# Optimization experiments

Hardware: AMD Instinct MI355X
Metric: run time of the kernel (lower is better)

Reference implementation:

```python
import jax, jax.numpy as jnp
import numpy as np

N = 50000
E = 800000
F_IN = 64
HID = 64


def setup_inputs() -> dict:
    key = jax.random.key(0)
    k1, k2, k3, k4, k5, k6 = jax.random.split(key, 6)
    x = jax.random.normal(k1, (N, F_IN), dtype=jnp.float32)
    edge_index = jax.random.randint(k2, (2, E), 0, N, dtype=jnp.int64)
    # GraphSAGE mean-aggregator layers: Linear(2*in -> out) applied to [x || mean_agg(x)]
    W1 = jax.random.normal(k3, (2 * F_IN, HID), dtype=jnp.float32) / np.sqrt(2 * F_IN)
    b1 = jnp.zeros((HID,), dtype=jnp.float32)
    W2 = jax.random.normal(k4, (2 * HID, HID), dtype=jnp.float32) / np.sqrt(2 * HID)
    b2 = jnp.zeros((HID,), dtype=jnp.float32)
    return {"x": x, "edge_index": edge_index, "W1": W1, "b1": b1, "W2": W2, "b2": b2}


def _sage_conv(x, src, dst, W, b):
    # mean aggregation of neighbor (src) features at dst, then linear on [self || agg]
    msg = x[src]                                                   # [E, d] gather
    s = jax.ops.segment_sum(msg, dst, num_segments=N)              # [N, d]
    cnt = jax.ops.segment_sum(jnp.ones((src.shape[0], 1), x.dtype), dst, num_segments=N)
    agg = s / jnp.maximum(cnt, 1.0)
    return jnp.concatenate([x, agg], axis=-1) @ W + b


def reference(x, edge_index, W1, b1, W2, b2):
    src, dst = edge_index[0], edge_index[1]
    h = _sage_conv(x, src, dst, W1, b1)
    h = jax.nn.relu(h)  # dropout is identity at inference
    h = _sage_conv(h, src, dst, W2, b2)
    return h
```

## Files before the change

kernel.cpp:

```cpp
#include <hip/hip_runtime.h>

#define N_NODES 50000
#define N_EDGES 800000
#define F 64
#define CHUNK 6144
#define NWG1 ((N_EDGES + CHUNK - 1) / CHUNK)
#define NBUCK 196
#define CAP2 8192
#define NWTILE (N_NODES / 16)

typedef __attribute__((ext_vector_type(8))) _Float16 half8;
typedef __attribute__((ext_vector_type(4))) float f32x4;

__global__ __launch_bounds__(256) void conv_hist(
    const float4* __restrict__ xin,
    half8*        __restrict__ x16,
    const int*    __restrict__ dst,
    int*          __restrict__ bhist,
    const float*  __restrict__ W1, const float* __restrict__ W2,
    _Float16*     __restrict__ Wt1, _Float16* __restrict__ Wt2) {
  int t = threadIdx.x, b = blockIdx.x;
  if (b == NWG1) {
    for (int i = t; i < 64 * 128; i += 256) {
      int n = i >> 7, k = i & 127;
      Wt1[i] = (_Float16)W1[k * 64 + n];
      Wt2[i] = (_Float16)W2[k * 64 + n];
    }
    return;
  }
  __shared__ int h[256];
  h[t] = 0; __syncthreads();
  int e0 = b * CHUNK;
  int cnt = N_EDGES - e0; if (cnt > CHUNK) cnt = CHUNK;
  for (int i = t; i < cnt; i += 256) atomicAdd(&h[dst[e0 + i] >> 8], 1);
  const int TOT = N_NODES * F / 8;
  for (int i = b * 256 + t; i < TOT; i += NWG1 * 256) {
    float4 a = xin[i * 2], c = xin[i * 2 + 1];
    half8 hh;
    hh[0] = (_Float16)a.x; hh[1] = (_Float16)a.y;
    hh[2] = (_Float16)a.z; hh[3] = (_Float16)a.w;
    hh[4] = (_Float16)c.x; hh[5] = (_Float16)c.y;
    hh[6] = (_Float16)c.z; hh[7] = (_Float16)c.w;
    x16[i] = hh;
  }
  __syncthreads();
  bhist[b * 256 + t] = h[t];
}

__global__ __launch_bounds__(256) void partition_det(
    const int* __restrict__ src, const int* __restrict__ dst,
    const int* __restrict__ bhist,
    int*       __restrict__ cstart_g,
    unsigned*  __restrict__ ebuf) {
  __shared__ int scn[256], gbase[256], lscan[256], lcur[256];
  __shared__ unsigned stage[CHUNK];
  int t = threadIdx.x, myb = blockIdx.x;

  int rowsum = 0, total = 0, mine = 0;
  for (int b = 0; b < NWG1; ++b) {
    int v = bhist[b * 256 + t];
    total += v;
    rowsum += (b < myb) ? v : 0;
    if (b == myb) mine = v;
  }
  scn[t] = total; __syncthreads();
  for (int off = 1; off < 256; off <<= 1) {
    int a = (t >= off) ? scn[t - off] : 0;
    __syncthreads();
    scn[t] += a;
    __syncthreads();
  }
  int cstart = scn[t] - total;
  gbase[t] = cstart + rowsum;
  if (myb == 0) {
    cstart_g[t] = cstart;
    if (t == 255) cstart_g[256] = scn[255];
  }

  lscan[t] = mine; __syncthreads();
  for (int off = 1; off < 256; off <<= 1) {
    int a = (t >= off) ? lscan[t - off] : 0;
    __syncthreads();
    lscan[t] += a;
    __syncthreads();
  }
  lscan[t] -= mine;
  lcur[t] = lscan[t];
  __syncthreads();

  int e0 = myb * CHUNK;
  int cnt = N_EDGES - e0; if (cnt > CHUNK) cnt = CHUNK;
  for (int i = t; i < cnt; i += 256) {
    int d = dst[e0 + i], s = src[e0 + i];
    int bb = d >> 8;
    int p = atomicAdd(&lcur[bb], 1);
    stage[p] = ((unsigned)bb << 24) | ((unsigned)(d & 255) << 16) | (unsigned)s;
  }
  __syncthreads();
  for (int i = t; i < cnt; i += 256) {
    unsigned e = stage[i];
    int bb = e >> 24;
    ebuf[gbase[bb] + (i - lscan[bb])] = e;
  }
}

__global__ __launch_bounds__(256) void bucket_sort(
    const unsigned* __restrict__ ebuf, const int* __restrict__ cstart,
    unsigned short* __restrict__ edge_src, int* __restrict__ row_start,
    int* __restrict__ deg) {
  __shared__ int lhist[256], lscan[256], lcur[256];
  __shared__ unsigned short srt[CAP2];
  int b = blockIdx.x, t = threadIdx.x;
  int s0 = cstart[b], s1 = cstart[b + 1];
  int cnt = s1 - s0;

  lhist[t] = 0; __syncthreads();
  for (int i = t; i < cnt; i += 256) atomicAdd(&lhist[(ebuf[s0 + i] >> 16) & 255], 1);
  __syncthreads();

  int v = lhist[t];
  lscan[t] = v; __syncthreads();
  for (int off = 1; off < 256; off <<= 1) {
    int a = (t >= off) ? lscan[t - off] : 0;
    __syncthreads();
    lscan[t] += a;
    __syncthreads();
  }
  lscan[t] -= v;
  lcur[t] = lscan[t];
  __syncthreads();

  for (int i = t; i < cnt; i += 256) {
    unsigned e = ebuf[s0 + i];
    int p = atomicAdd(&lcur[(e >> 16) & 255], 1);
    srt[p] = (unsigned short)(e & 0xFFFFu);
  }
  __syncthreads();

  for (int i = t; i < cnt; i += 256) edge_src[s0 + i] = srt[i];

  int n = b * 256 + t;
  if (n < N_NODES) { row_start[n] = s0 + lscan[t]; deg[n] = v; }
}

__global__ __launch_bounds__(256) void sage_layer_fused(
    const half8*    __restrict__ feat16,
    const _Float16* __restrict__ self16,
    const int*      __restrict__ row_start,
    const int*      __restrict__ deg,
    const unsigned short* __restrict__ edge_src,
    const _Float16* __restrict__ Wt,
    const float*    __restrict__ bias,
    float*          __restrict__ outf,
    unsigned short* __restrict__ out16,
    int do_relu) {
  __shared__ _Float16 lmean[32 * 72];
  int t = threadIdx.x;
  int w = t >> 6, lane = t & 63;

  {
    int o = lane >> 3, q = lane & 7;
    int n = blockIdx.x * 32 + w * 8 + o;
    if (n < N_NODES) {
      int start = row_start[n];
      int d     = deg[n];
      float a0=0.f,a1=0.f,a2=0.f,a3=0.f,a4=0.f,a5=0.f,a6=0.f,a7=0.f;
      for (int base = 0; base < d; base += 8) {
        #pragma unroll
        for (int uu = 0; uu < 8; ++uu) {
          int e = base + uu;
          if (e < d) {
            int s = (int)edge_src[start + e];
            half8 v = feat16[(size_t)s * 8 + q];
            a0 += (float)v[0]; a1 += (float)v[1]; a2 += (float)v[2]; a3 += (float)v[3];
            a4 += (float)v[4]; a5 += (float)v[5]; a6 += (float)v[6]; a7 += (float)v[7];
          }
        }
      }
      float inv = (d > 0) ? 1.0f / (float)d : 0.0f;
      half8 h;
      h[0] = (_Float16)(a0*inv); h[1] = (_Float16)(a1*inv);
      h[2] = (_Float16)(a2*inv); h[3] = (_Float16)(a3*inv);
      h[4] = (_Float16)(a4*inv); h[5] = (_Float16)(a5*inv);
      h[6] = (_Float16)(a6*inv); h[7] = (_Float16)(a7*inv);
      *(half8*)&lmean[(w * 8 + o) * 72 + q * 8] = h;
    }
  }
  __syncthreads();

  int tile = w >> 1;
  int wt = blockIdx.x * 2 + tile;
  if (wt >= NWTILE) return;
  int m = lane & 15, quad = lane >> 4;
  size_t arow = (size_t)(wt * 16 + m) * 64 + quad * 8;
  half8 a0 = *(const half8*)(self16 + arow);
  half8 a1 = *(const half8*)(self16 + arow + 32);
  int ln = tile * 16 + m;
  half8 a2 = *(const half8*)&lmean[ln * 72 + quad * 8];
  half8 a3 = *(const half8*)&lmean[ln * 72 + quad * 8 + 32];

  int nt0 = (w & 1) * 2;
  #pragma unroll
  for (int i = 0; i < 2; ++i) {
    int nt = nt0 + i;
    float bv = bias[nt * 16 + m];
    f32x4 acc = (f32x4){bv, bv, bv, bv};
    const _Float16* wrow = Wt + (size_t)(nt * 16 + m) * 128 + quad * 8;
    half8 b0 = *(const half8*)(wrow);
    half8 b1 = *(const half8*)(wrow + 32);
    half8 b2 = *(const half8*)(wrow + 64);
    half8 b3 = *(const half8*)(wrow + 96);
    acc = __builtin_amdgcn_mfma_f32_16x16x32_f16(a0, b0, acc, 0, 0, 0);
    acc = __builtin_amdgcn_mfma_f32_16x16x32_f16(a1, b1, acc, 0, 0, 0);
    acc = __builtin_amdgcn_mfma_f32_16x16x32_f16(a2, b2, acc, 0, 0, 0);
    acc = __builtin_amdgcn_mfma_f32_16x16x32_f16(a3, b3, acc, 0, 0, 0);
    #pragma unroll
    for (int r = 0; r < 4; ++r) {
      size_t off = (size_t)(wt * 16 + quad * 4 + r) * 64 + nt * 16 + m;
      float v = acc[r];
      if (do_relu) v = fmaxf(v, 0.0f);
      if (outf)  outf[off] = v;
      if (out16) { _Float16 hv = (_Float16)v; out16[off] = *(unsigned short*)&hv; }
    }
  }
}

extern "C" void kernel_launch(void* const* d_in, const int* in_sizes, int n_in,
                              void* d_out, int out_size, void* d_ws, size_t ws_size,
                              hipStream_t stream) {
  const float* x  = (const float*)d_in[0];
  const int*   ei = (const int*)d_in[1];
  const float* W1 = (const float*)d_in[2];
  const float* b1 = (const float*)d_in[3];
  const float* W2 = (const float*)d_in[4];
  const float* b2 = (const float*)d_in[5];
  float* out = (float*)d_out;

  const int* src = ei;
  const int* dst = ei + N_EDGES;

  int* wsi       = (int*)d_ws;
  int* bhist     = wsi;
  int* cstart    = wsi + 33824;
  int* deg       = wsi + 34112;
  int* row_start = wsi + 84160;
  unsigned short* edge_src = (unsigned short*)(wsi + 134208);
  unsigned* ebuf = (unsigned*)(wsi + 534208);
  half8* x16     = (half8*)(wsi + 1334208);
  unsigned short* h116 = (unsigned short*)(wsi + 2934208);
  _Float16* Wt1  = (_Float16*)(wsi + 6134208);
  _Float16* Wt2  = (_Float16*)(wsi + 6138304);

  dim3 blk(256);
  conv_hist<<<NWG1 + 1, blk, 0, stream>>>(
      (const float4*)x, x16, dst, bhist, W1, W2, Wt1, Wt2);
  partition_det<<<NWG1, blk, 0, stream>>>(src, dst, bhist, cstart, ebuf);
  bucket_sort<<<NBUCK, blk, 0, stream>>>(ebuf, cstart, edge_src, row_start, deg);

  dim3 grd_fused((N_NODES + 31) / 32);

  sage_layer_fused<<<grd_fused, blk, 0, stream>>>(
      x16, (const _Float16*)x16, row_start, deg, edge_src,
      Wt1, b1, nullptr, h116, 1);
  sage_layer_fused<<<grd_fused, blk, 0, stream>>>(
      (const half8*)h116, (const _Float16*)h116, row_start, deg, edge_src,
      Wt2, b2, out, nullptr, 0);
}
```

Measured before the change: 168.7 us.

## Merge histogram and partition kernels using atomic per-bucket offsets in fixed-stride buffers

Fuses the histogram/convert kernel with the partition kernel. Each workgroup now claims space in a fixed-stride per-bucket region through a global atomic counter, so the cross-workgroup prefix scan over all block histograms goes away. This removes one kernel launch and the serial read of the whole histogram table, but adds a memset and makes the order of edges within a bucket nondeterministic. It also assumes no bucket ever holds more than 8192 edges.

```diff
diff --git a/kernel.cpp b/kernel.cpp
--- a/kernel.cpp
+++ b/kernel.cpp
@@ -6,19 +6,20 @@
 #define CHUNK 6144
 #define NWG1 ((N_EDGES + CHUNK - 1) / CHUNK)
 #define NBUCK 196
-#define CAP2 8192
+#define BSTRIDE 8192
 #define NWTILE (N_NODES / 16)
 
 typedef __attribute__((ext_vector_type(8))) _Float16 half8;
 typedef __attribute__((ext_vector_type(4))) float f32x4;
 
-__global__ __launch_bounds__(256) void conv_hist(
+__global__ __launch_bounds__(256) void partition_conv(
+    const int*    __restrict__ src, const int* __restrict__ dst,
     const float4* __restrict__ xin,
     half8*        __restrict__ x16,
-    const int*    __restrict__ dst,
-    int*          __restrict__ bhist,
     const float*  __restrict__ W1, const float* __restrict__ W2,
-    _Float16*     __restrict__ Wt1, _Float16* __restrict__ Wt2) {
+    _Float16*     __restrict__ Wt1, _Float16* __restrict__ Wt2,
+    unsigned*     __restrict__ bcur,
+    unsigned*     __restrict__ ebuf) {
   int t = threadIdx.x, b = blockIdx.x;
   if (b == NWG1) {
     for (int i = t; i < 64 * 128; i += 256) {
@@ -28,11 +29,13 @@
     }
     return;
   }
-  __shared__ int h[256];
-  h[t] = 0; __syncthreads();
+  __shared__ int hist[256], lscan[256], lcur[256], gbase[256];
+  __shared__ unsigned stage[CHUNK];
+  hist[t] = 0; __syncthreads();
   int e0 = b * CHUNK;
   int cnt = N_EDGES - e0; if (cnt > CHUNK) cnt = CHUNK;
-  for (int i = t; i < cnt; i += 256) atomicAdd(&h[dst[e0 + i] >> 8], 1);
+  for (int i = t; i < cnt; i += 256) atomicAdd(&hist[dst[e0 + i] >> 8], 1);
+
   const int TOT = N_NODES * F / 8;
   for (int i = b * 256 + t; i < TOT; i += NWG1 * 256) {
     float4 a = xin[i * 2], c = xin[i * 2 + 1];
@@ -44,52 +47,20 @@
     x16[i] = hh;
   }
   __syncthreads();
-  bhist[b * 256 + t] = h[t];
-}
-
-__global__ __launch_bounds__(256) void partition_det(
-    const int* __restrict__ src, const int* __restrict__ dst,
-    const int* __restrict__ bhist,
-    int*       __restrict__ cstart_g,
-    unsigned*  __restrict__ ebuf) {
-  __shared__ int scn[256], gbase[256], lscan[256], lcur[256];
-  __shared__ unsigned stage[CHUNK];
-  int t = threadIdx.x, myb = blockIdx.x;
-
-  int rowsum = 0, total = 0, mine = 0;
-  for (int b = 0; b < NWG1; ++b) {
-    int v = bhist[b * 256 + t];
-    total += v;
-    rowsum += (b < myb) ? v : 0;
-    if (b == myb) mine = v;
-  }
-  scn[t] = total; __syncthreads();
-  for (int off = 1; off < 256; off <<= 1) {
-    int a = (t >= off) ? scn[t - off] : 0;
-    __syncthreads();
-    scn[t] += a;
-    __syncthreads();
-  }
-  int cstart = scn[t] - total;
-  gbase[t] = cstart + rowsum;
-  if (myb == 0) {
-    cstart_g[t] = cstart;
-    if (t == 255) cstart_g[256] = scn[255];
-  }
-
-  lscan[t] = mine; __syncthreads();
+
+  int v = hist[t];
+  lscan[t] = v; __syncthreads();
   for (int off = 1; off < 256; off <<= 1) {
     int a = (t >= off) ? lscan[t - off] : 0;
     __syncthreads();
     lscan[t] += a;
     __syncthreads();
   }
-  lscan[t] -= mine;
+  lscan[t] -= v;
   lcur[t] = lscan[t];
-  __syncthreads();
-
-  int e0 = myb * CHUNK;
-  int cnt = N_EDGES - e0; if (cnt > CHUNK) cnt = CHUNK;
+  if (v > 0) gbase[t] = (int)atomicAdd(&bcur[t], (unsigned)v);
+  __syncthreads();
+
   for (int i = t; i < cnt; i += 256) {
     int d = dst[e0 + i], s = src[e0 + i];
     int bb = d >> 8;
@@ -100,19 +71,19 @@
   for (int i = t; i < cnt; i += 256) {
     unsigned e = stage[i];
     int bb = e >> 24;
-    ebuf[gbase[bb] + (i - lscan[bb])] = e;
+    ebuf[bb * BSTRIDE + gbase[bb] + (i - lscan[bb])] = e;
   }
 }
 
 __global__ __launch_bounds__(256) void bucket_sort(
-    const unsigned* __restrict__ ebuf, const int* __restrict__ cstart,
+    const unsigned* __restrict__ ebuf, const unsigned* __restrict__ bcur,
     unsigned short* __restrict__ edge_src, int* __restrict__ row_start,
     int* __restrict__ deg) {
   __shared__ int lhist[256], lscan[256], lcur[256];
-  __shared__ unsigned short srt[CAP2];
+  __shared__ unsigned short srt[BSTRIDE];
   int b = blockIdx.x, t = threadIdx.x;
-  int s0 = cstart[b], s1 = cstart[b + 1];
-  int cnt = s1 - s0;
+  int s0 = b * BSTRIDE;
+  int cnt = (int)bcur[b];
 
   lhist[t] = 0; __syncthreads();
   for (int i = t; i < cnt; i += 256) atomicAdd(&lhist[(ebuf[s0 + i] >> 16) & 255], 1);
@@ -240,22 +211,22 @@
   const int* dst = ei + N_EDGES;
 
   int* wsi       = (int*)d_ws;
-  int* bhist     = wsi;
-  int* cstart    = wsi + 33824;
-  int* deg       = wsi + 34112;
-  int* row_start = wsi + 84160;
-  unsigned short* edge_src = (unsigned short*)(wsi + 134208);
-  unsigned* ebuf = (unsigned*)(wsi + 534208);
-  half8* x16     = (half8*)(wsi + 1334208);
-  unsigned short* h116 = (unsigned short*)(wsi + 2934208);
-  _Float16* Wt1  = (_Float16*)(wsi + 6134208);
-  _Float16* Wt2  = (_Float16*)(wsi + 6138304);
+  unsigned* bcur = (unsigned*)wsi;
+  int* deg       = wsi + 256;
+  int* row_start = wsi + 50304;
+  unsigned short* edge_src = (unsigned short*)(wsi + 100352);
+  unsigned* ebuf = (unsigned*)(wsi + 903168);
+  half8* x16     = (half8*)(wsi + 2508800);
+  unsigned short* h116 = (unsigned short*)(wsi + 4108800);
+  _Float16* Wt1  = (_Float16*)(wsi + 5708800);
+  _Float16* Wt2  = (_Float16*)(wsi + 5712896);
+
+  hipMemsetAsync(bcur, 0, 256 * sizeof(unsigned), stream);
 
   dim3 blk(256);
-  conv_hist<<<NWG1 + 1, blk, 0, stream>>>(
-      (const float4*)x, x16, dst, bhist, W1, W2, Wt1, Wt2);
-  partition_det<<<NWG1, blk, 0, stream>>>(src, dst, bhist, cstart, ebuf);
-  bucket_sort<<<NBUCK, blk, 0, stream>>>(ebuf, cstart, edge_src, row_start, deg);
+  partition_conv<<<NWG1 + 1, blk, 0, stream>>>(
+      src, dst, (const float4*)x, x16, W1, W2, Wt1, Wt2, bcur, ebuf);
+  bucket_sort<<<NBUCK, blk, 0, stream>>>(ebuf, bcur, edge_src, row_start, deg);
 
   dim3 grd_fused((N_NODES + 31) / 32);
 
```

Result: faster. 160.4 us (-4.9%).
